# Kernel optimization log

Hardware: AMD Instinct MI355X
Metric: run time of the kernel (lower is better)

## Reference

```python
import jax, jax.numpy as jnp
import numpy as np

N = 6144          # atoms (~300 residues)
K = 6             # sequence-separation bins (k_vals clamped to 0..5)
T = 85            # RASP 'all' atom types
D = 21            # distance bins -> max_d = 20 A
NBRE_NT_EXCLU = 2 # exclude pairs with residue separation <= 2
N_RES = 307


def setup_inputs() -> dict:
    key = jax.random.key(0)
    k1, k2, k3, k4, k5 = jax.random.split(key, 5)
    # coords scaled so pair distances populate the 0..20 A bin range
    coords = jax.random.normal(k1, (N, 3), jnp.float32) * 5.0
    # atoms grouped by residue -> sorted residue ids
    res_ids = jnp.sort(jax.random.randint(k2, (N,), 0, N_RES)).astype(jnp.int32)
    types = jax.random.randint(k3, (N,), 0, T).astype(jnp.int32)
    types = jnp.where(jax.random.uniform(k4, (N,)) < 0.02, jnp.int32(-1), types)
    pot_tensor = jax.random.normal(k5, (K, T, T, D), jnp.float32) * 0.5
    return {"coords": coords, "res_ids": res_ids, "types": types, "pot_tensor": pot_tensor}


def reference(coords, res_ids, types, pot_tensor):
    n = coords.shape[0]
    # static upper-triangular pair indices (i < j), as in torch.triu_indices(offset=1)
    ii_np, jj_np = np.triu_indices(n, k=1)
    ii = jnp.asarray(ii_np, jnp.int32)
    jj = jnp.asarray(jj_np, jnp.int32)

    sep = jnp.abs(res_ids[ii] - res_ids[jj])                       # [P]
    mask = (sep > NBRE_NT_EXCLU) & (types[ii] != -1) & (types[jj] != -1)

    diff = coords[ii] - coords[jj]                                 # [P,3]
    dists = jnp.sqrt(jnp.sum(diff * diff, axis=1)) + 1e-8          # [P]

    k_vals = jnp.clip(sep - 1, 0, 5)
    max_d = pot_tensor.shape[3] - 1
    d0 = jnp.floor(jnp.clip(dists, 0, max_d)).astype(jnp.int32)
    d1 = jnp.minimum(d0 + 1, max_d)
    alpha = dists - d0.astype(dists.dtype)

    # masked pairs may carry type -1; redirect their gather to index 0
    # (their contribution is zeroed by `mask` below, matching torch semantics)
    ti = jnp.where(mask, types[ii], 0)
    tj = jnp.where(mask, types[jj], 0)

    e0 = pot_tensor[k_vals, ti, tj, d0]                            # [P] 4D gather
    e1 = pot_tensor[k_vals, ti, tj, d1]

    contrib = ((1.0 - alpha) * e0 + alpha * e1 - 2.7)
    contrib = contrib * (dists < max_d).astype(contrib.dtype) * mask.astype(contrib.dtype)
    return jnp.sum(contrib)
```

## Files before the change

### kernel.cpp

```cpp
#include <hip/hip_runtime.h>


#define T_TYPES 85
#define D_BINS 21
#define TSTRIDE (T_TYPES * D_BINS)
#define KSTRIDE (T_TYPES * T_TYPES * D_BINS)
#define INVALID_KEY 85
#define NKEYS 86
#define TILE 128
#define PAIR_THREADS 512
#define JCHUNK 32

__global__ __launch_bounds__(1024) void sort_kernel(const float* __restrict__ coords,
                                                    const int* __restrict__ res_ids,
                                                    const int* __restrict__ types, int n,
                                                    float4* __restrict__ sorted,
                                                    float* __restrict__ out) {
    __shared__ int hist[NKEYS];
    __shared__ int offs[NKEYS];
    int tid = threadIdx.x;
    if (tid < NKEYS) hist[tid] = 0;
    if (tid == 0) *out = 0.0f;
    __syncthreads();
    for (int i = tid; i < n; i += 1024) {
        int t = types[i];
        int key = (t < 0) ? INVALID_KEY : t;
        atomicAdd(&hist[key], 1);
    }
    __syncthreads();
    if (tid == 0) {
        int s = 0;
        for (int i = 0; i < NKEYS; ++i) { offs[i] = s; s += hist[i]; }
    }
    __syncthreads();
    for (int i = tid; i < n; i += 1024) {
        int t = types[i];
        int key = (t < 0) ? INVALID_KEY : t;
        int pos = atomicAdd(&offs[key], 1);
        float4 v;
        v.x = coords[3 * i + 0];
        v.y = coords[3 * i + 1];
        v.z = coords[3 * i + 2];
        v.w = __int_as_float((res_ids[i] << 7) | key);
        sorted[pos] = v;
    }
}

__global__ __launch_bounds__(PAIR_THREADS) void pair_kernel(const float4* __restrict__ sorted,
                                                            const float* __restrict__ pot,
                                                            int n, int nt,
                                                            float* __restrict__ out) {
    __shared__ float4 jtile[TILE];
    __shared__ float wsum[PAIR_THREADS / 64];

    int b = blockIdx.x;
    int bi = (int)((2.0 * nt + 1.0 -
                    sqrt((2.0 * nt + 1.0) * (2.0 * nt + 1.0) - 8.0 * (double)b)) * 0.5);
    if (bi < 0) bi = 0;
    if (bi > nt - 1) bi = nt - 1;
    while ((bi + 1) * nt - ((bi + 1) * bi) / 2 <= b) ++bi;
    while (bi * nt - (bi * (bi - 1)) / 2 > b) --bi;
    int bj = bi + (b - (bi * nt - (bi * (bi - 1)) / 2));

    int tid = threadIdx.x;
    int ilane = tid & (TILE - 1);
    int chunk = tid >> 7;
    int q0 = bj * TILE;

    if (tid < TILE) {
        int q = q0 + tid;
        float4 v;
        if (q < n) v = sorted[q];
        else { v.x = 0.f; v.y = 0.f; v.z = 0.f; v.w = __int_as_float(INVALID_KEY); }
        jtile[tid] = v;
    }
    __syncthreads();

    int p = bi * TILE + ilane;
    float4 mine;
    if (p < n) mine = sorted[p];
    else { mine.x = 0.f; mine.y = 0.f; mine.z = 0.f; mine.w = __int_as_float(INVALID_KEY); }

    int packi = __float_as_int(mine.w);
    int keyi = packi & 127;
    int resi = packi >> 7;
    int vi = (keyi < INVALID_KEY) ? 1 : 0;
    int tbase = keyi * TSTRIDE;

    float acc = 0.0f;
    int j0 = chunk * JCHUNK;
#pragma unroll 8
    for (int u = 0; u < JCHUNK; ++u) {
        int jj = j0 + u;
        float4 o = jtile[jj];
        int q = q0 + jj;
        float dx = mine.x - o.x;
        float dy = mine.y - o.y;
        float dz = mine.z - o.z;
        float d2 = dx * dx + dy * dy + dz * dz;
        float dist = __builtin_amdgcn_sqrtf(d2) + 1e-8f;

        int packj = __float_as_int(o.w);
        int keyj = packj & 127;
        int resj = packj >> 7;
        int sep = resi - resj;
        sep = (sep < 0) ? -sep : sep;

        int valid = (q > p) & vi & (keyj < INVALID_KEY) & (sep > 2) & (dist < 20.0f);

        int k = sep - 1;
        k = (k < 0) ? 0 : k;
        k = (k > 5) ? 5 : k;

        int d0 = (int)dist;
        d0 = (d0 > 19) ? 19 : d0;
        float alpha = dist - (float)d0;

        int idx = k * KSTRIDE + tbase + keyj * D_BINS + d0;
        idx = valid ? idx : 0;
        float e0 = pot[idx];
        float e1 = pot[idx + 1];
        float val = __builtin_fmaf(alpha, e1 - e0, e0) - 2.7f;
        acc += valid ? val : 0.0f;
    }

#pragma unroll
    for (int off = 32; off > 0; off >>= 1)
        acc += __shfl_down(acc, off, 64);
    int wave = tid >> 6;
    int lane = tid & 63;
    if (lane == 0) wsum[wave] = acc;
    __syncthreads();
    if (tid == 0) {
        float s = 0.f;
#pragma unroll
        for (int w = 0; w < PAIR_THREADS / 64; ++w) s += wsum[w];
        atomicAdd(out, s);
    }
}

extern "C" void kernel_launch(void* const* d_in, const int* in_sizes, int n_in,
                              void* d_out, int out_size, void* d_ws, size_t ws_size,
                              hipStream_t stream) {
    const float* coords = (const float*)d_in[0];
    const int* res_ids = (const int*)d_in[1];
    const int* types   = (const int*)d_in[2];
    const float* pot   = (const float*)d_in[3];
    int n = in_sizes[1];
    float* out = (float*)d_out;

    float4* sorted = (float4*)d_ws;

    sort_kernel<<<1, 1024, 0, stream>>>(coords, res_ids, types, n, sorted, out);

    int nt = (n + TILE - 1) / TILE;
    int nblocks = nt * (nt + 1) / 2;
    pair_kernel<<<nblocks, PAIR_THREADS, 0, stream>>>(sorted, pot, n, nt, out);
}
```

Before: 91.73 us.

## Stage per-tile potential slice in shared memory and encode invalid atoms as far-away points

Each pair block computes the type range its i and j tiles cover, which is narrow because atoms are sorted by type. When that range fits, it copies the matching slice of the potential table (all 6 separation bins) into shared memory so the inner loop's two-value gathers hit LDS instead of global memory. Blocks with a wide type range fall back to global gathers. Invalid-type and padding atoms are now placed at huge coordinates so the distance cutoff removes them, which drops the per-pair type-validity checks. The cost is the extra staging work per block, more shared memory, and two code paths.

```diff
diff --git a/kernel.cpp b/kernel.cpp
--- a/kernel.cpp
+++ b/kernel.cpp
@@ -8,8 +8,9 @@
 #define INVALID_KEY 85
 #define NKEYS 86
 #define TILE 128
-#define PAIR_THREADS 512
-#define JCHUNK 32
+#define PTHREADS 512
+#define JCHUNK (TILE / (PTHREADS / TILE))
+#define MAXSLOTS 36
 
 __global__ __launch_bounds__(1024) void sort_kernel(const float* __restrict__ coords,
                                                     const int* __restrict__ res_ids,
@@ -24,8 +25,7 @@
     __syncthreads();
     for (int i = tid; i < n; i += 1024) {
         int t = types[i];
-        int key = (t < 0) ? INVALID_KEY : t;
-        atomicAdd(&hist[key], 1);
+        atomicAdd(&hist[(t < 0) ? INVALID_KEY : t], 1);
     }
     __syncthreads();
     if (tid == 0) {
@@ -38,20 +38,27 @@
         int key = (t < 0) ? INVALID_KEY : t;
         int pos = atomicAdd(&offs[key], 1);
         float4 v;
-        v.x = coords[3 * i + 0];
-        v.y = coords[3 * i + 1];
-        v.z = coords[3 * i + 2];
-        v.w = __int_as_float((res_ids[i] << 7) | key);
+        if (t < 0) {
+            v.x = 1.0e6f + 1000.0f * (float)pos;
+            v.y = 0.0f; v.z = 0.0f;
+            v.w = __int_as_float((res_ids[i] << 7) | 84);
+        } else {
+            v.x = coords[3 * i + 0];
+            v.y = coords[3 * i + 1];
+            v.z = coords[3 * i + 2];
+            v.w = __int_as_float((res_ids[i] << 7) | t);
+        }
         sorted[pos] = v;
     }
 }
 
-__global__ __launch_bounds__(PAIR_THREADS) void pair_kernel(const float4* __restrict__ sorted,
-                                                            const float* __restrict__ pot,
-                                                            int n, int nt,
-                                                            float* __restrict__ out) {
+__global__ __launch_bounds__(PTHREADS) void pair_kernel(const float4* __restrict__ sorted,
+                                                        const float* __restrict__ pot,
+                                                        int n, int nt,
+                                                        float* __restrict__ out) {
     __shared__ float4 jtile[TILE];
-    __shared__ float wsum[PAIR_THREADS / 64];
+    __shared__ float pot_s[6 * MAXSLOTS * D_BINS];
+    __shared__ float wsum[PTHREADS / 64];
 
     int b = blockIdx.x;
     int bi = (int)((2.0 * nt + 1.0 -
@@ -65,63 +72,110 @@
     int tid = threadIdx.x;
     int ilane = tid & (TILE - 1);
     int chunk = tid >> 7;
-    int q0 = bj * TILE;
+    int i0 = bi * TILE, q0 = bj * TILE;
+
+    int ihi = min(i0 + TILE, n) - 1;
+    int jhi = min(q0 + TILE, n) - 1;
+    int tloi = min(__float_as_int(sorted[i0].w) & 127, 84);
+    int thii = min(__float_as_int(sorted[ihi].w) & 127, 84);
+    int tloj = min(__float_as_int(sorted[q0].w) & 127, 84);
+    int thij = min(__float_as_int(sorted[jhi].w) & 127, 84);
+    int nti = thii - tloi + 1;
+    int ntj = thij - tloj + 1;
+    int slots = nti * ntj;
+    bool staged = (slots <= MAXSLOTS);
 
     if (tid < TILE) {
         int q = q0 + tid;
         float4 v;
         if (q < n) v = sorted[q];
-        else { v.x = 0.f; v.y = 0.f; v.z = 0.f; v.w = __int_as_float(INVALID_KEY); }
+        else { v.x = 3.0e7f; v.y = 0.f; v.z = 0.f; v.w = __int_as_float(0); }
         jtile[tid] = v;
     }
-    __syncthreads();
-
-    int p = bi * TILE + ilane;
+
+    if (staged) {
+        int total = 6 * slots * D_BINS;
+        for (int e = tid; e < total; e += PTHREADS) {
+            int d = e % D_BINS;
+            int s2 = e / D_BINS;
+            int slot = s2 % slots;
+            int k = s2 / slots;
+            int tii = slot / ntj;
+            int tjj = slot - tii * ntj;
+            pot_s[e] = pot[k * KSTRIDE + (tloi + tii) * TSTRIDE + (tloj + tjj) * D_BINS + d];
+        }
+    }
+    __syncthreads();
+
+    int p = i0 + ilane;
     float4 mine;
     if (p < n) mine = sorted[p];
-    else { mine.x = 0.f; mine.y = 0.f; mine.z = 0.f; mine.w = __int_as_float(INVALID_KEY); }
-
-    int packi = __float_as_int(mine.w);
-    int keyi = packi & 127;
-    int resi = packi >> 7;
-    int vi = (keyi < INVALID_KEY) ? 1 : 0;
-    int tbase = keyi * TSTRIDE;
+    else { mine.x = 2.0e7f; mine.y = 0.f; mine.z = 0.f; mine.w = __int_as_float(0); }
+
+    int pki = __float_as_int(mine.w);
+    int keyi = pki & 127;
+    int resi = pki >> 7;
+    int islot = min(max(keyi - tloi, 0), nti - 1);
+    int sbase = islot * ntj;
+    int tibase_g = min(keyi, 84) * TSTRIDE;
+    int pjb = p - q0;
 
     float acc = 0.0f;
     int j0 = chunk * JCHUNK;
+
+    if (staged) {
 #pragma unroll 8
-    for (int u = 0; u < JCHUNK; ++u) {
-        int jj = j0 + u;
-        float4 o = jtile[jj];
-        int q = q0 + jj;
-        float dx = mine.x - o.x;
-        float dy = mine.y - o.y;
-        float dz = mine.z - o.z;
-        float d2 = dx * dx + dy * dy + dz * dz;
-        float dist = __builtin_amdgcn_sqrtf(d2) + 1e-8f;
-
-        int packj = __float_as_int(o.w);
-        int keyj = packj & 127;
-        int resj = packj >> 7;
-        int sep = resi - resj;
-        sep = (sep < 0) ? -sep : sep;
-
-        int valid = (q > p) & vi & (keyj < INVALID_KEY) & (sep > 2) & (dist < 20.0f);
-
-        int k = sep - 1;
-        k = (k < 0) ? 0 : k;
-        k = (k > 5) ? 5 : k;
-
-        int d0 = (int)dist;
-        d0 = (d0 > 19) ? 19 : d0;
-        float alpha = dist - (float)d0;
-
-        int idx = k * KSTRIDE + tbase + keyj * D_BINS + d0;
-        idx = valid ? idx : 0;
-        float e0 = pot[idx];
-        float e1 = pot[idx + 1];
-        float val = __builtin_fmaf(alpha, e1 - e0, e0) - 2.7f;
-        acc += valid ? val : 0.0f;
+        for (int u = 0; u < JCHUNK; ++u) {
+            int jj = j0 + u;
+            float4 o = jtile[jj];
+            float dx = mine.x - o.x;
+            float dy = mine.y - o.y;
+            float dz = mine.z - o.z;
+            float d2 = dx * dx + dy * dy + dz * dz;
+            float dist = __builtin_amdgcn_sqrtf(d2);
+
+            int pkj = __float_as_int(o.w);
+            int keyj = pkj & 127;
+            int resj = pkj >> 7;
+            int sep = abs(resi - resj);
+            int jslot = min(max(keyj - tloj, 0), ntj - 1);
+            int k = min(max(sep - 1, 0), 5);
+            int d0i = min((int)dist, 19);
+            float alpha = dist - (float)d0i;
+
+            int li = (k * slots + sbase + jslot) * D_BINS + d0i;
+            float e0 = pot_s[li];
+            float e1 = pot_s[li + 1];
+            float val = __builtin_fmaf(alpha, e1 - e0, e0) - 2.7f;
+            bool valid = (sep > 2) && (dist < 20.0f) && (jj > pjb);
+            acc += valid ? val : 0.0f;
+        }
+    } else {
+#pragma unroll 4
+        for (int u = 0; u < JCHUNK; ++u) {
+            int jj = j0 + u;
+            float4 o = jtile[jj];
+            float dx = mine.x - o.x;
+            float dy = mine.y - o.y;
+            float dz = mine.z - o.z;
+            float d2 = dx * dx + dy * dy + dz * dz;
+            float dist = __builtin_amdgcn_sqrtf(d2);
+
+            int pkj = __float_as_int(o.w);
+            int keyj = min(pkj & 127, 84);
+            int resj = pkj >> 7;
+            int sep = abs(resi - resj);
+            int k = min(max(sep - 1, 0), 5);
+            int d0i = min((int)dist, 19);
+            float alpha = dist - (float)d0i;
+
+            int gi = k * KSTRIDE + tibase_g + keyj * D_BINS + d0i;
+            float e0 = pot[gi];
+            float e1 = pot[gi + 1];
+            float val = __builtin_fmaf(alpha, e1 - e0, e0) - 2.7f;
+            bool valid = (sep > 2) && (dist < 20.0f) && (jj > pjb);
+            acc += valid ? val : 0.0f;
+        }
     }
 
 #pragma unroll
@@ -134,7 +188,7 @@
     if (tid == 0) {
         float s = 0.f;
 #pragma unroll
-        for (int w = 0; w < PAIR_THREADS / 64; ++w) s += wsum[w];
+        for (int w = 0; w < PTHREADS / 64; ++w) s += wsum[w];
         atomicAdd(out, s);
     }
 }
@@ -155,5 +209,5 @@
 
     int nt = (n + TILE - 1) / TILE;
     int nblocks = nt * (nt + 1) / 2;
-    pair_kernel<<<nblocks, PAIR_THREADS, 0, stream>>>(sorted, pot, n, nt, out);
+    pair_kernel<<<nblocks, PTHREADS, 0, stream>>>(sorted, pot, n, nt, out);
 }
```

Measured after the change: 94.02 us. 1.02x slower.
